# Optimization experiments

Hardware: AMD Instinct MI355X
Metric: run time of the kernel (lower is better)

## Reference

```python
import jax, jax.numpy as jnp
import numpy as np

NUM_LABELS_I = 28  # 7 entity types * 4 (B/I/E/S)
NUM_LABELS = 31    # + O, EOS, BOS
INDEX_O, INDEX_EOS, INDEX_BOS = 28, 29, 30
NEG = -10000.0


def _make_trans(rng):
    # replicate ChainCRF4NestedNER.reset_parameters() structural masking
    bs = np.arange(0, NUM_LABELS_I, 4)
    is_ = bs + 1
    es = bs + 2
    ss = bs + 3
    t = (rng.standard_normal((NUM_LABELS, NUM_LABELS)) * 0.1).astype(np.float32)
    for i in bs:
        t[i, :i + 1] = NEG; t[i, i + 3:] = NEG
    for i in is_:
        t[i, :i] = NEG; t[i, i + 2:] = NEG
    for i in np.concatenate([es, ss, [INDEX_O]]):
        t[i, is_] = NEG; t[i, es] = NEG; t[i, INDEX_BOS] = NEG
    t[INDEX_EOS, :INDEX_EOS] = NEG; t[INDEX_EOS, INDEX_BOS] = NEG
    t[INDEX_BOS, is_] = NEG; t[INDEX_BOS, es] = NEG; t[INDEX_BOS, INDEX_BOS] = NEG
    return jnp.asarray(t)


def setup_inputs() -> dict:
    B, T, D = 64, 512, 768
    key = jax.random.key(0)
    k1, k2, k3 = jax.random.split(key, 3)
    inp = jax.random.normal(k1, (B, T, D), dtype=jnp.float32)
    target = jax.random.randint(k2, (B, T), 0, 29, dtype=jnp.int64)  # real labels + O only
    mask = jnp.ones((B, T), dtype=jnp.float32)
    state_w = jax.random.normal(k3, (NUM_LABELS, D), dtype=jnp.float32) * 0.02
    state_b = jnp.concatenate([jnp.zeros(INDEX_EOS, jnp.float32),
                               jnp.full(NUM_LABELS - INDEX_EOS, NEG, jnp.float32)])
    trans = _make_trans(np.random.default_rng(0))
    return {"input": inp, "target": target, "mask": mask,
            "state_w": state_w, "state_b": state_b, "trans": trans}


def reference(input, target, mask, state_w, state_b, trans):
    B, T, _ = input.shape
    # state scores [B, T, L]
    out_s = jnp.einsum('btd,ld->btl', input, state_w) + state_b
    out_s = out_s.at[:, :, INDEX_EOS].add((mask == 0).astype(out_s.dtype) * 20000.0)
    # energy [B, T, L, L]: trans[prev, curr] + state[curr]
    energy = trans[None, None, :, :] + out_s[:, :, None, :]
    # forward algorithm (logsumexp semiring) as a scan over time
    energy_t = jnp.moveaxis(energy, 1, 0)  # [T, B, L, L]
    part0 = energy_t[0, :, INDEX_BOS, :]   # [B, L]

    def step(part, e_t):
        new = jax.nn.logsumexp(e_t + part[:, :, None], axis=1)
        return new, None

    partition, _ = jax.lax.scan(step, part0, energy_t[1:])
    # gold-path energy: sum_t energy[b, t, prev_label, label]
    prev = jnp.concatenate([jnp.full((B, 1), INDEX_BOS, dtype=target.dtype),
                            target[:, :-1]], axis=1)
    bi = jnp.arange(B)[:, None]
    ti = jnp.arange(T)[None, :]
    tgt_energy = energy[bi, ti, prev, target].sum(axis=1)
    loss = jax.nn.logsumexp(trans[:, INDEX_EOS][None, :] + partition, axis=1) - tgt_energy
    return loss, energy
```

## Files before the change

kernel.cpp:

```cpp
#include <hip/hip_runtime.h>

typedef float f32x4  __attribute__((ext_vector_type(4)));
typedef float f32x16 __attribute__((ext_vector_type(16)));
typedef short s16x8  __attribute__((ext_vector_type(8)));

constexpr int NL  = 31;
constexpr int BB  = 64;
constexpr int TT  = 512;
constexpr int DD  = 768;
constexpr int RTOT = BB * TT;
constexpr int IDX_EOS = 29;
constexpr int IDX_BOS = 30;
constexpr float LOG2E = 1.4426950408889634f;
constexpr float LN2F  = 0.6931471805599453f;

union Frag8 { unsigned u[4]; s16x8 s; };

__device__ inline unsigned pk2(float a, float b) {
  unsigned ua = __float_as_uint(a), ub = __float_as_uint(b);
  ua = (ua + 0x7fffu + ((ua >> 16) & 1u)) >> 16;
  ub = (ub + 0x7fffu + ((ub >> 16) & 1u)) >> 16;
  return ua | (ub << 16);
}
__device__ inline unsigned short bf16r(float a) {
  unsigned ua = __float_as_uint(a);
  return (unsigned short)((ua + 0x7fffu + ((ua >> 16) & 1u)) >> 16);
}

__device__ inline float bfly_max32(float v) {
#define STEPM(K) { float o = __int_as_float(__builtin_amdgcn_ds_swizzle(__float_as_int(v), ((K) << 10) | 0x1f)); v = fmaxf(v, o); }
  STEPM(1) STEPM(2) STEPM(4) STEPM(8) STEPM(16)
#undef STEPM
  return v;
}
__device__ inline float bfly_sum32(float v) {
#define STEPS(K) { float o = __int_as_float(__builtin_amdgcn_ds_swizzle(__float_as_int(v), ((K) << 10) | 0x1f)); v = v + o; }
  STEPS(1) STEPS(2) STEPS(4) STEPS(8) STEPS(16)
#undef STEPS
  return v;
}

__device__ inline void repack(const float E[16], int h, Frag8& B1, Frag8& B2) {
  unsigned o1a = pk2(E[4 * h], E[4 * h + 1]), o1b = pk2(E[4 * h + 2], E[4 * h + 3]);
  unsigned o2a = pk2(E[8 + 4 * h], E[8 + 4 * h + 1]), o2b = pk2(E[8 + 4 * h + 2], E[8 + 4 * h + 3]);
  int hb = 4 * (1 - h);
  unsigned s1a = pk2(E[hb], E[hb + 1]),         s1b = pk2(E[hb + 2], E[hb + 3]);
  unsigned s2a = pk2(E[8 + hb], E[8 + hb + 1]), s2b = pk2(E[8 + hb + 2], E[8 + hb + 3]);
  unsigned r1a = __shfl_xor((int)s1a, 32), r1b = __shfl_xor((int)s1b, 32);
  unsigned r2a = __shfl_xor((int)s2a, 32), r2b = __shfl_xor((int)s2b, 32);
  if (h == 0) {
    B1.u[0] = o1a; B1.u[1] = o1b; B1.u[2] = r1a; B1.u[3] = r1b;
    B2.u[0] = o2a; B2.u[1] = o2b; B2.u[2] = r2a; B2.u[3] = r2b;
  } else {
    B1.u[0] = r1a; B1.u[1] = r1b; B1.u[2] = o1a; B1.u[3] = o1b;
    B2.u[0] = r2a; B2.u[1] = r2b; B2.u[2] = o2a; B2.u[3] = o2b;
  }
}

__device__ inline void renorm16(float E[16], float& Sacc) {
  float m = E[0];
#pragma unroll
  for (int r = 1; r < 16; ++r) m = fmaxf(m, E[r]);
  m = bfly_max32(m);
  m = fmaxf(m, __shfl_xor(m, 32));
  float lg = truncf(log2f(m));
  Sacc += lg;
  float sc = exp2f(-lg);
#pragma unroll
  for (int r = 0; r < 16; ++r) E[r] *= sc;
}

__device__ inline void load_A16(const unsigned short* M, int l, int h, Frag8& A1, Frag8& A2) {
  A1.s = *(const s16x8*)(M + l * 32 + 8 * h);
  A2.s = *(const s16x8*)(M + l * 32 + 16 + 8 * h);
}
__device__ inline void load_B16(const unsigned short* M, int l, int h, Frag8& B1, Frag8& B2) {
#pragma unroll
  for (int m = 0; m < 4; ++m) {
    int k = 8 * h + 2 * m;
    unsigned lo0 = M[k * 32 + l],        hi0 = M[(k + 1) * 32 + l];
    unsigned lo1 = M[(k + 16) * 32 + l], hi1 = M[(k + 17) * 32 + l];
    B1.u[m] = lo0 | (hi0 << 16);
    B2.u[m] = lo1 | (hi1 << 16);
  }
}

__global__ void k_prep(const float* __restrict__ sw, unsigned short* __restrict__ Bw,
                       float* __restrict__ ws_tgt) {
  if (blockIdx.x == 0 && threadIdx.x < BB) ws_tgt[threadIdx.x] = 0.f;
  for (int i = blockIdx.x * 256 + threadIdx.x; i < 32 * DD; i += 8 * 256)
    Bw[i] = (i < NL * DD) ? bf16r(sw[i]) : (unsigned short)0;
}

__global__ __launch_bounds__(256) void k_outs(
    const float* __restrict__ inp, const unsigned short* __restrict__ Bw,
    const float* __restrict__ sb, const float* __restrict__ msk,
    float* __restrict__ outs)
{
  __shared__ unsigned short As[4][16 * 72];
  int tid = threadIdx.x, wave = tid >> 6, lane = tid & 63;
  int quad = lane >> 4, l15 = lane & 15;
  int r0 = blockIdx.x * 64 + wave * 16;
  int srow = lane >> 2, scol = lane & 3;
  const float* gsrc = inp + (size_t)(r0 + srow) * DD + scol * 4;
  unsigned short* asb = As[wave];
  unsigned* dw = (unsigned*)asb;
  int wbase = srow * 36 + scol * 2;

  f32x4 pre[4];
#pragma unroll
  for (int i = 0; i < 4; ++i) pre[i] = *(const f32x4*)(gsrc + i * 16);

  f32x4 acc[2] = {};
  for (int kc = 0; kc < 12; ++kc) {
#pragma unroll
    for (int i = 0; i < 4; ++i) {
      dw[wbase + i * 8]     = pk2(pre[i][0], pre[i][1]);
      dw[wbase + i * 8 + 1] = pk2(pre[i][2], pre[i][3]);
    }
    if (kc < 11) {
      const float* g2 = gsrc + (kc + 1) * 64;
#pragma unroll
      for (int i = 0; i < 4; ++i) pre[i] = *(const f32x4*)(g2 + i * 16);
    }
#pragma unroll
    for (int ks = 0; ks < 2; ++ks) {
      s16x8 af = *(const s16x8*)(asb + l15 * 72 + ks * 32 + quad * 8);
#pragma unroll
      for (int ct = 0; ct < 2; ++ct) {
        s16x8 bf = *(const s16x8*)(Bw + (ct * 16 + l15) * DD + kc * 64 + ks * 32 + quad * 8);
        acc[ct] = __builtin_amdgcn_mfma_f32_16x16x32_bf16(af, bf, acc[ct], 0, 0, 0);
      }
    }
  }
#pragma unroll
  for (int ct = 0; ct < 2; ++ct) {
    int n = ct * 16 + l15;
    if (n >= NL) continue;
    float b = sb[n];
#pragma unroll
    for (int r = 0; r < 4; ++r) {
      int row = r0 + quad * 4 + r;
      float v = acc[ct][r] + b;
      if (n == IDX_EOS && msk[row] == 0.f) v += 20000.f;
      outs[(size_t)row * NL + n] = v;
    }
  }
}

__global__ __launch_bounds__(256) void k_main(
    const float* __restrict__ outs, const float* __restrict__ trans,
    const int* __restrict__ target, float* __restrict__ energy,
    unsigned short* __restrict__ Mseg16, float* __restrict__ Sseg,
    float* __restrict__ ws_tgt)
{
  __shared__ float smem[961 + 64 * NL];
  int bid = blockIdx.x;
  int tid = threadIdx.x, wave = tid >> 6, lane = tid & 63;

  if (bid < 1024) {
    int l = lane & 31, h = lane >> 5;
    int unit = bid * 4 + wave;
    int b = unit >> 6, c = unit & 63;
    int t0 = 1 + c * 8;
    int n = (c == 63) ? 7 : 8;

    float* ub = smem + wave * 256;
#pragma unroll
    for (int it = 0; it < 4; ++it) {
      int idx = lane + it * 64;
      int row = idx >> 5, col = idx & 31;
      float v = 0.f;
      if (col < NL && row < n)
        v = exp2f(LOG2E * outs[((size_t)b * TT + t0 + row) * NL + col]);
      ub[idx] = v;
    }
    __syncthreads();

    Frag8 A1, A2, B1, B2;
#pragma unroll
    for (int m = 0; m < 4; ++m) {
      int k0 = 8 * h + 2 * m, k1 = k0 + 1;
      float a0 = (k0 < NL && l < NL) ? exp2f(LOG2E * trans[k0 * NL + l]) : 0.f;
      float a1 = (k1 < NL && l < NL) ? exp2f(LOG2E * trans[k1 * NL + l]) : 0.f;
      A1.u[m] = pk2(a0, a1);
      int k2 = 16 + k0, k3 = 16 + k1;
      float a2 = (k2 < NL && l < NL) ? exp2f(LOG2E * trans[k2 * NL + l]) : 0.f;
      float a3 = (k3 < NL && l < NL) ? exp2f(LOG2E * trans[k3 * NL + l]) : 0.f;
      A2.u[m] = pk2(a2, a3);
      B1.u[m] = ((k0 == l) ? 0x3f80u : 0u) | (((k1 == l) ? 0x3f80u : 0u) << 16);
      B2.u[m] = ((k2 == l) ? 0x3f80u : 0u) | (((k3 == l) ? 0x3f80u : 0u) << 16);
    }

    float E[16];
    for (int s = 0; s < n; ++s) {
      const float* us = ub + s * 32 + 4 * h;
      f32x4 u0 = *(const f32x4*)(us);
      f32x4 u1 = *(const f32x4*)(us + 8);
      f32x4 u2 = *(const f32x4*)(us + 16);
      f32x4 u3 = *(const f32x4*)(us + 24);
      f32x16 D = {};
      D = __builtin_amdgcn_mfma_f32_32x32x16_bf16(A1.s, B1.s, D, 0, 0, 0);
      D = __builtin_amdgcn_mfma_f32_32x32x16_bf16(A2.s, B2.s, D, 0, 0, 0);
#pragma unroll
      for (int jj = 0; jj < 4; ++jj) {
        E[jj]      = D[jj]      * u0[jj];
        E[4 + jj]  = D[4 + jj]  * u1[jj];
        E[8 + jj]  = D[8 + jj]  * u2[jj];
        E[12 + jj] = D[12 + jj] * u3[jj];
      }
      if (s + 1 < n) repack(E, h, B1, B2);
    }
    float S = 0.f;
    renorm16(E, S);
    unsigned short* mo = Mseg16 + (size_t)unit * 1024;
#pragma unroll
    for (int r = 0; r < 16; ++r) {
      int row = (r & 3) + 8 * (r >> 2) + 4 * h;
      mo[row * 32 + l] = bf16r(E[r]);
    }
    if (lane == 0) Sseg[unit] = S;
    return;
  }

  int r0 = (bid - 1024) * 64;
  float* tr  = smem;
  float* osh = smem + 961;
  for (int idx = tid; idx < 961; idx += 256) tr[idx] = trans[idx];
  for (int idx = tid; idx < 64 * NL; idx += 256)
    osh[idx] = outs[(size_t)r0 * NL + idx];
  __syncthreads();

  if (tid < 64) {
    int r = r0 + tid;
    int tg = target[r];
    int prv = ((r & (TT - 1)) == 0) ? IDX_BOS : target[r - 1];
    float cc = tr[prv * NL + tg] + osh[tid * NL + tg];
#pragma unroll
    for (int off = 32; off; off >>= 1) cc += __shfl_down(cc, off);
    if (tid == 0) atomicAdd(&ws_tgt[r0 / TT], cc);
  }

  float* dst = energy + (size_t)r0 * 961;
#pragma unroll 4
  for (int it = 0; it < 60; ++it) {
    int v = it * 256 + tid;
    int e = v * 4;
    f32x4 val;
#pragma unroll
    for (int k = 0; k < 4; ++k) {
      unsigned x = e + k;
      unsigned q = __umulhi(x, 4469269u);
      unsigned c = x - q * 961u;
      unsigned j = c - 31u * ((c * 67651u) >> 21);
      val[k] = tr[c] + osh[q * NL + j];
    }
    *(f32x4*)(dst + e) = val;
  }
  if (tid < 16) {
    int e = (15360 + tid) * 4;
    f32x4 val;
#pragma unroll
    for (int k = 0; k < 4; ++k) {
      unsigned x = e + k;
      unsigned q = __umulhi(x, 4469269u);
      unsigned c = x - q * 961u;
      unsigned j = c - 31u * ((c * 67651u) >> 21);
      val[k] = tr[c] + osh[q * NL + j];
    }
    *(f32x4*)(dst + e) = val;
  }
}

__global__ __launch_bounds__(256) void k_tree1(
    const unsigned short* __restrict__ Mseg16, const float* __restrict__ Sseg,
    unsigned short* __restrict__ Mq16, float* __restrict__ Sq)
{
  int tid = threadIdx.x, wave = tid >> 6, lane = tid & 63;
  int l = lane & 31, h = lane >> 5;
  int unit = blockIdx.x * 4 + wave;
  const unsigned short* base = Mseg16 + (size_t)unit * 4096;
  Frag8 A1, A2, B1, B2;
  load_B16(base, l, h, B1, B2);
  float S = Sseg[unit * 4] + Sseg[unit * 4 + 1] + Sseg[unit * 4 + 2] + Sseg[unit * 4 + 3];
  float E[16];
#pragma unroll
  for (int i = 1; i < 4; ++i) {
    load_A16(base + i * 1024, l, h, A1, A2);
    f32x16 D = {};
    D = __builtin_amdgcn_mfma_f32_32x32x16_bf16(A1.s, B1.s, D, 0, 0, 0);
    D = __builtin_amdgcn_mfma_f32_32x32x16_bf16(A2.s, B2.s, D, 0, 0, 0);
#pragma unroll
    for (int r = 0; r < 16; ++r) E[r] = D[r];
    if (i < 3) repack(E, h, B1, B2);
  }
  renorm16(E, S);
  unsigned short* mo = Mq16 + (size_t)unit * 1024;
#pragma unroll
  for (int r = 0; r < 16; ++r) {
    int row = (r & 3) + 8 * (r >> 2) + 4 * h;
    mo[row * 32 + l] = bf16r(E[r]);
  }
  if (lane == 0) Sq[unit] = S;
}

__global__ __launch_bounds__(256) void k_tree2(
    const float* __restrict__ outs, const float* __restrict__ trans,
    const unsigned short* __restrict__ Mq16, const float* __restrict__ Sq,
    const float* __restrict__ ws_tgt, float* __restrict__ loss)
{
  int tid = threadIdx.x, wave = tid >> 6, lane = tid & 63;
  int l = lane & 31, h = lane >> 5;
  int b = blockIdx.x * 4 + wave;
  const unsigned short* base = Mq16 + (size_t)b * 16384;
  Frag8 A1, A2, B1, B2;
  load_B16(base, l, h, B1, B2);
  float S = 0.f;
#pragma unroll
  for (int q = 0; q < 16; ++q) S += Sq[b * 16 + q];
  float E[16];
  for (int i = 1; i < 16; ++i) {
    load_A16(base + i * 1024, l, h, A1, A2);
    f32x16 D = {};
    D = __builtin_amdgcn_mfma_f32_32x32x16_bf16(A1.s, B1.s, D, 0, 0, 0);
    D = __builtin_amdgcn_mfma_f32_32x32x16_bf16(A2.s, B2.s, D, 0, 0, 0);
#pragma unroll
    for (int r = 0; r < 16; ++r) E[r] = D[r];
    if ((i & 3) == 3) renorm16(E, S);
    if (i < 15) repack(E, h, B1, B2);
  }
  float p0 = (l < NL) ? exp2f(LOG2E * (trans[IDX_BOS * NL + l] + outs[(size_t)b * TT * NL + l])) : 0.f;
  float sum_h = 0.f;
#pragma unroll
  for (int r = 0; r < 16; ++r) {
    float s = bfly_sum32(E[r] * p0);
    int row = (r & 3) + 8 * (r >> 2) + 4 * h;
    float We = (row < NL) ? exp2f(LOG2E * trans[row * NL + IDX_EOS]) : 0.f;
    sum_h += s * We;
  }
  float tot = sum_h + __shfl_xor(sum_h, 32);
  if (lane == 0) loss[b] = LN2F * (S + log2f(tot)) - ws_tgt[b];
}

extern "C" void kernel_launch(void* const* d_in, const int* in_sizes, int n_in,
                              void* d_out, int out_size, void* d_ws, size_t ws_size,
                              hipStream_t stream) {
  const float* inp   = (const float*)d_in[0];
  const int*   tgt   = (const int*)d_in[1];
  const float* msk   = (const float*)d_in[2];
  const float* sw    = (const float*)d_in[3];
  const float* sb    = (const float*)d_in[4];
  const float* trans = (const float*)d_in[5];

  float* out    = (float*)d_out;
  float* loss   = out;
  float* energy = out + BB;

  float* outs   = (float*)d_ws;
  float* Sseg   = outs + (size_t)RTOT * NL;
  float* Sq     = Sseg + 4096;
  float* ws_tgt = Sq + 1024;
  unsigned short* Mseg16 = (unsigned short*)(ws_tgt + 64);
  unsigned short* Mq16   = Mseg16 + (size_t)4096 * 1024;
  unsigned short* Bw     = Mq16 + (size_t)1024 * 1024;

  k_prep<<<8, 256, 0, stream>>>(sw, Bw, ws_tgt);
  k_outs<<<RTOT / 64, 256, 0, stream>>>(inp, Bw, sb, msk, outs);
  k_main<<<1536, 256, 0, stream>>>(outs, trans, tgt, energy, Mseg16, Sseg, ws_tgt);
  k_tree1<<<256, 256, 0, stream>>>(Mseg16, Sseg, Mq16, Sq);
  k_tree2<<<16, 256, 0, stream>>>(outs, trans, Mq16, Sq, ws_tgt, loss);
}
```

Measured before the change: 301.5 us.

## Fuse energy write into GEMM kernel and merge segment scan with first tree level

The energy-tensor write and the gold-path partial sums move into the state-score GEMM kernel. That kernel now keeps its 64x31 tile and the transition matrix in shared memory, so it no longer re-reads outs from global memory. The per-segment transfer-matrix scan is merged with the first 4-way tree reduction in one kernel that combines in shared memory, which removes the Mseg16 global round trip and one launch. Atomics on the target energy are replaced by per-block partials summed in the final kernel, which also drops the zeroing in k_prep. The risk is that the GEMM kernel's tail gets longer, and the segment and energy phases no longer run concurrently in one grid.

Result: no change. 305.5 us (+1.3%).

```diff
diff --git a/kernel.cpp b/kernel.cpp
--- a/kernel.cpp
+++ b/kernel.cpp
@@ -85,9 +85,7 @@
   }
 }
 
-__global__ void k_prep(const float* __restrict__ sw, unsigned short* __restrict__ Bw,
-                       float* __restrict__ ws_tgt) {
-  if (blockIdx.x == 0 && threadIdx.x < BB) ws_tgt[threadIdx.x] = 0.f;
+__global__ void k_prep(const float* __restrict__ sw, unsigned short* __restrict__ Bw) {
   for (int i = blockIdx.x * 256 + threadIdx.x; i < 32 * DD; i += 8 * 256)
     Bw[i] = (i < NL * DD) ? bf16r(sw[i]) : (unsigned short)0;
 }
@@ -95,14 +93,22 @@
 __global__ __launch_bounds__(256) void k_outs(
     const float* __restrict__ inp, const unsigned short* __restrict__ Bw,
     const float* __restrict__ sb, const float* __restrict__ msk,
-    float* __restrict__ outs)
+    const float* __restrict__ trans, const int* __restrict__ target,
+    float* __restrict__ outs, float* __restrict__ energy,
+    float* __restrict__ ws_partial)
 {
-  __shared__ unsigned short As[4][16 * 72];
+  __shared__ __align__(16) unsigned short As[4][16 * 72];
+  __shared__ float tr[961];
+  __shared__ float osh[64 * NL];
   int tid = threadIdx.x, wave = tid >> 6, lane = tid & 63;
   int quad = lane >> 4, l15 = lane & 15;
-  int r0 = blockIdx.x * 64 + wave * 16;
+  int r0 = blockIdx.x * 64;
+  int rw = r0 + wave * 16;
+
+  for (int idx = tid; idx < 961; idx += 256) tr[idx] = trans[idx];
+
   int srow = lane >> 2, scol = lane & 3;
-  const float* gsrc = inp + (size_t)(r0 + srow) * DD + scol * 4;
+  const float* gsrc = inp + (size_t)(rw + srow) * DD + scol * 4;
   unsigned short* asb = As[wave];
   unsigned* dw = (unsigned*)asb;
   int wbase = srow * 36 + scol * 2;
@@ -140,95 +146,14 @@
     float b = sb[n];
 #pragma unroll
     for (int r = 0; r < 4; ++r) {
-      int row = r0 + quad * 4 + r;
+      int lr = wave * 16 + quad * 4 + r;
+      int row = r0 + lr;
       float v = acc[ct][r] + b;
       if (n == IDX_EOS && msk[row] == 0.f) v += 20000.f;
+      osh[lr * NL + n] = v;
       outs[(size_t)row * NL + n] = v;
     }
   }
-}
-
-__global__ __launch_bounds__(256) void k_main(
-    const float* __restrict__ outs, const float* __restrict__ trans,
-    const int* __restrict__ target, float* __restrict__ energy,
-    unsigned short* __restrict__ Mseg16, float* __restrict__ Sseg,
-    float* __restrict__ ws_tgt)
-{
-  __shared__ float smem[961 + 64 * NL];
-  int bid = blockIdx.x;
-  int tid = threadIdx.x, wave = tid >> 6, lane = tid & 63;
-
-  if (bid < 1024) {
-    int l = lane & 31, h = lane >> 5;
-    int unit = bid * 4 + wave;
-    int b = unit >> 6, c = unit & 63;
-    int t0 = 1 + c * 8;
-    int n = (c == 63) ? 7 : 8;
-
-    float* ub = smem + wave * 256;
-#pragma unroll
-    for (int it = 0; it < 4; ++it) {
-      int idx = lane + it * 64;
-      int row = idx >> 5, col = idx & 31;
-      float v = 0.f;
-      if (col < NL && row < n)
-        v = exp2f(LOG2E * outs[((size_t)b * TT + t0 + row) * NL + col]);
-      ub[idx] = v;
-    }
-    __syncthreads();
-
-    Frag8 A1, A2, B1, B2;
-#pragma unroll
-    for (int m = 0; m < 4; ++m) {
-      int k0 = 8 * h + 2 * m, k1 = k0 + 1;
-      float a0 = (k0 < NL && l < NL) ? exp2f(LOG2E * trans[k0 * NL + l]) : 0.f;
-      float a1 = (k1 < NL && l < NL) ? exp2f(LOG2E * trans[k1 * NL + l]) : 0.f;
-      A1.u[m] = pk2(a0, a1);
-      int k2 = 16 + k0, k3 = 16 + k1;
-      float a2 = (k2 < NL && l < NL) ? exp2f(LOG2E * trans[k2 * NL + l]) : 0.f;
-      float a3 = (k3 < NL && l < NL) ? exp2f(LOG2E * trans[k3 * NL + l]) : 0.f;
-      A2.u[m] = pk2(a2, a3);
-      B1.u[m] = ((k0 == l) ? 0x3f80u : 0u) | (((k1 == l) ? 0x3f80u : 0u) << 16);
-      B2.u[m] = ((k2 == l) ? 0x3f80u : 0u) | (((k3 == l) ? 0x3f80u : 0u) << 16);
-    }
-
-    float E[16];
-    for (int s = 0; s < n; ++s) {
-      const float* us = ub + s * 32 + 4 * h;
-      f32x4 u0 = *(const f32x4*)(us);
-      f32x4 u1 = *(const f32x4*)(us + 8);
-      f32x4 u2 = *(const f32x4*)(us + 16);
-      f32x4 u3 = *(const f32x4*)(us + 24);
-      f32x16 D = {};
-      D = __builtin_amdgcn_mfma_f32_32x32x16_bf16(A1.s, B1.s, D, 0, 0, 0);
-      D = __builtin_amdgcn_mfma_f32_32x32x16_bf16(A2.s, B2.s, D, 0, 0, 0);
-#pragma unroll
-      for (int jj = 0; jj < 4; ++jj) {
-        E[jj]      = D[jj]      * u0[jj];
-        E[4 + jj]  = D[4 + jj]  * u1[jj];
-        E[8 + jj]  = D[8 + jj]  * u2[jj];
-        E[12 + jj] = D[12 + jj] * u3[jj];
-      }
-      if (s + 1 < n) repack(E, h, B1, B2);
-    }
-    float S = 0.f;
-    renorm16(E, S);
-    unsigned short* mo = Mseg16 + (size_t)unit * 1024;
-#pragma unroll
-    for (int r = 0; r < 16; ++r) {
-      int row = (r & 3) + 8 * (r >> 2) + 4 * h;
-      mo[row * 32 + l] = bf16r(E[r]);
-    }
-    if (lane == 0) Sseg[unit] = S;
-    return;
-  }
-
-  int r0 = (bid - 1024) * 64;
-  float* tr  = smem;
-  float* osh = smem + 961;
-  for (int idx = tid; idx < 961; idx += 256) tr[idx] = trans[idx];
-  for (int idx = tid; idx < 64 * NL; idx += 256)
-    osh[idx] = outs[(size_t)r0 * NL + idx];
   __syncthreads();
 
   if (tid < 64) {
@@ -238,7 +163,7 @@
     float cc = tr[prv * NL + tg] + osh[tid * NL + tg];
 #pragma unroll
     for (int off = 32; off; off >>= 1) cc += __shfl_down(cc, off);
-    if (tid == 0) atomicAdd(&ws_tgt[r0 / TT], cc);
+    if (tid == 0) ws_partial[blockIdx.x] = cc;
   }
 
   float* dst = energy + (size_t)r0 * 961;
@@ -272,42 +197,105 @@
   }
 }
 
-__global__ __launch_bounds__(256) void k_tree1(
-    const unsigned short* __restrict__ Mseg16, const float* __restrict__ Sseg,
+__global__ __launch_bounds__(256) void k_seg(
+    const float* __restrict__ outs, const float* __restrict__ trans,
     unsigned short* __restrict__ Mq16, float* __restrict__ Sq)
 {
+  __shared__ float ub4[4][256];
+  __shared__ __align__(16) unsigned short Ms[4][1024];
+  __shared__ float Ss[4];
   int tid = threadIdx.x, wave = tid >> 6, lane = tid & 63;
   int l = lane & 31, h = lane >> 5;
   int unit = blockIdx.x * 4 + wave;
-  const unsigned short* base = Mseg16 + (size_t)unit * 4096;
+  int b = unit >> 6, c = unit & 63;
+  int t0 = 1 + c * 8;
+  int n = (c == 63) ? 7 : 8;
+
+  float* ub = ub4[wave];
+#pragma unroll
+  for (int it = 0; it < 4; ++it) {
+    int idx = lane + it * 64;
+    int row = idx >> 5, col = idx & 31;
+    float v = 0.f;
+    if (col < NL && row < n)
+      v = exp2f(LOG2E * outs[((size_t)b * TT + t0 + row) * NL + col]);
+    ub[idx] = v;
+  }
+
   Frag8 A1, A2, B1, B2;
-  load_B16(base, l, h, B1, B2);
-  float S = Sseg[unit * 4] + Sseg[unit * 4 + 1] + Sseg[unit * 4 + 2] + Sseg[unit * 4 + 3];
+#pragma unroll
+  for (int m = 0; m < 4; ++m) {
+    int k0 = 8 * h + 2 * m, k1 = k0 + 1;
+    float a0 = (k0 < NL && l < NL) ? exp2f(LOG2E * trans[k0 * NL + l]) : 0.f;
+    float a1 = (k1 < NL && l < NL) ? exp2f(LOG2E * trans[k1 * NL + l]) : 0.f;
+    A1.u[m] = pk2(a0, a1);
+    int k2 = 16 + k0, k3 = 16 + k1;
+    float a2 = (k2 < NL && l < NL) ? exp2f(LOG2E * trans[k2 * NL + l]) : 0.f;
+    float a3 = (k3 < NL && l < NL) ? exp2f(LOG2E * trans[k3 * NL + l]) : 0.f;
+    A2.u[m] = pk2(a2, a3);
+    B1.u[m] = ((k0 == l) ? 0x3f80u : 0u) | (((k1 == l) ? 0x3f80u : 0u) << 16);
+    B2.u[m] = ((k2 == l) ? 0x3f80u : 0u) | (((k3 == l) ? 0x3f80u : 0u) << 16);
+  }
+
   float E[16];
-#pragma unroll
-  for (int i = 1; i < 4; ++i) {
-    load_A16(base + i * 1024, l, h, A1, A2);
+  for (int s = 0; s < n; ++s) {
+    const float* us = ub + s * 32 + 4 * h;
+    f32x4 u0 = *(const f32x4*)(us);
+    f32x4 u1 = *(const f32x4*)(us + 8);
+    f32x4 u2 = *(const f32x4*)(us + 16);
+    f32x4 u3 = *(const f32x4*)(us + 24);
     f32x16 D = {};
     D = __builtin_amdgcn_mfma_f32_32x32x16_bf16(A1.s, B1.s, D, 0, 0, 0);
     D = __builtin_amdgcn_mfma_f32_32x32x16_bf16(A2.s, B2.s, D, 0, 0, 0);
 #pragma unroll
-    for (int r = 0; r < 16; ++r) E[r] = D[r];
-    if (i < 3) repack(E, h, B1, B2);
-  }
+    for (int jj = 0; jj < 4; ++jj) {
+      E[jj]      = D[jj]      * u0[jj];
+      E[4 + jj]  = D[4 + jj]  * u1[jj];
+      E[8 + jj]  = D[8 + jj]  * u2[jj];
+      E[12 + jj] = D[12 + jj] * u3[jj];
+    }
+    if (s + 1 < n) repack(E, h, B1, B2);
+  }
+  float S = 0.f;
   renorm16(E, S);
-  unsigned short* mo = Mq16 + (size_t)unit * 1024;
+  unsigned short* mo = Ms[wave];
 #pragma unroll
   for (int r = 0; r < 16; ++r) {
     int row = (r & 3) + 8 * (r >> 2) + 4 * h;
     mo[row * 32 + l] = bf16r(E[r]);
   }
-  if (lane == 0) Sq[unit] = S;
+  if (lane == 0) Ss[wave] = S;
+  __syncthreads();
+
+  if (wave == 0) {
+    load_B16(Ms[0], l, h, B1, B2);
+    float Sx = Ss[0] + Ss[1] + Ss[2] + Ss[3];
+    float E2[16];
+#pragma unroll
+    for (int i = 1; i < 4; ++i) {
+      load_A16(Ms[i], l, h, A1, A2);
+      f32x16 D = {};
+      D = __builtin_amdgcn_mfma_f32_32x32x16_bf16(A1.s, B1.s, D, 0, 0, 0);
+      D = __builtin_amdgcn_mfma_f32_32x32x16_bf16(A2.s, B2.s, D, 0, 0, 0);
+#pragma unroll
+      for (int r = 0; r < 16; ++r) E2[r] = D[r];
+      if (i < 3) repack(E2, h, B1, B2);
+    }
+    renorm16(E2, Sx);
+    unsigned short* qo = Mq16 + (size_t)blockIdx.x * 1024;
+#pragma unroll
+    for (int r = 0; r < 16; ++r) {
+      int row = (r & 3) + 8 * (r >> 2) + 4 * h;
+      qo[row * 32 + l] = bf16r(E2[r]);
+    }
+    if (lane == 0) Sq[blockIdx.x] = Sx;
+  }
 }
 
 __global__ __launch_bounds__(256) void k_tree2(
     const float* __restrict__ outs, const float* __restrict__ trans,
     const unsigned short* __restrict__ Mq16, const float* __restrict__ Sq,
-    const float* __restrict__ ws_tgt, float* __restrict__ loss)
+    const float* __restrict__ ws_partial, float* __restrict__ loss)
 {
   int tid = threadIdx.x, wave = tid >> 6, lane = tid & 63;
   int l = lane & 31, h = lane >> 5;
@@ -339,7 +327,12 @@
     sum_h += s * We;
   }
   float tot = sum_h + __shfl_xor(sum_h, 32);
-  if (lane == 0) loss[b] = LN2F * (S + log2f(tot)) - ws_tgt[b];
+  if (lane == 0) {
+    float wst = 0.f;
+#pragma unroll
+    for (int i = 0; i < 8; ++i) wst += ws_partial[b * 8 + i];
+    loss[b] = LN2F * (S + log2f(tot)) - wst;
+  }
 }
 
 extern "C" void kernel_launch(void* const* d_in, const int* in_sizes, int n_in,
@@ -356,17 +349,14 @@
   float* loss   = out;
   float* energy = out + BB;
 
-  float* outs   = (float*)d_ws;
-  float* Sseg   = outs + (size_t)RTOT * NL;
-  float* Sq     = Sseg + 4096;
-  float* ws_tgt = Sq + 1024;
-  unsigned short* Mseg16 = (unsigned short*)(ws_tgt + 64);
-  unsigned short* Mq16   = Mseg16 + (size_t)4096 * 1024;
-  unsigned short* Bw     = Mq16 + (size_t)1024 * 1024;
-
-  k_prep<<<8, 256, 0, stream>>>(sw, Bw, ws_tgt);
-  k_outs<<<RTOT / 64, 256, 0, stream>>>(inp, Bw, sb, msk, outs);
-  k_main<<<1536, 256, 0, stream>>>(outs, trans, tgt, energy, Mseg16, Sseg, ws_tgt);
-  k_tree1<<<256, 256, 0, stream>>>(Mseg16, Sseg, Mq16, Sq);
-  k_tree2<<<16, 256, 0, stream>>>(outs, trans, Mq16, Sq, ws_tgt, loss);
-}
+  float* outs        = (float*)d_ws;
+  float* Sq          = outs + (size_t)RTOT * NL;
+  float* ws_partial  = Sq + 1024;
+  unsigned short* Mq16 = (unsigned short*)(ws_partial + 512);
+  unsigned short* Bw   = Mq16 + (size_t)1024 * 1024;
+
+  k_prep<<<8, 256, 0, stream>>>(sw, Bw);
+  k_outs<<<RTOT / 64, 256, 0, stream>>>(inp, Bw, sb, msk, trans, tgt, outs, energy, ws_partial);
+  k_seg<<<1024, 256, 0, stream>>>(outs, trans, Mq16, Sq);
+  k_tree2<<<16, 256, 0, stream>>>(outs, trans, Mq16, Sq, ws_partial, loss);
+}
```
